# Kernel optimization log

Hardware: AMD Instinct MI355X
Metric: run time of the kernel (lower is better)

Reference implementation:

```python
import jax, jax.numpy as jnp
import numpy as np

D_MODEL = 512
D_K = 64
D_V = 128
H = D_MODEL // D_V  # 4 heads (num_head = d_model // d_v per the source)
B, N = 4, 2048


def setup_inputs() -> dict:
    key = jax.random.key(0)
    k0, k1, k2, k3, k4 = jax.random.split(key, 5)
    s = 0.02
    return {
        "input_x": jax.random.normal(k0, (B, N, D_MODEL), jnp.float32),
        "Wq": jax.random.normal(k1, (D_MODEL, H * D_K), jnp.float32) * s,
        "Wk": jax.random.normal(k2, (D_MODEL, H * D_K), jnp.float32) * s,
        "Wv": jax.random.normal(k3, (D_MODEL, D_MODEL), jnp.float32) * s,
        "Wo": jax.random.normal(k4, (D_MODEL, D_MODEL), jnp.float32) * s,
    }


def reference(input_x, Wq, Wk, Wv, Wo):
    b, n, _ = input_x.shape
    # Contiguous per-head slices in the source == a simple reshape here.
    q = (input_x @ Wq).reshape(b, n, H, D_K)   # [B,N,H,dk]
    k = (input_x @ Wk).reshape(b, n, H, D_K)   # [B,N,H,dk]
    v = (input_x @ Wv).reshape(b, n, H, D_V)   # [B,N,H,dv]
    scale = jnp.sqrt(jnp.float32(D_K))
    scores = jnp.einsum('bqhd,bkhd->bhqk', q, k) / scale  # [B,H,N,N]
    # FAITHFUL quirk: the source uses nn.Softmax() with no dim on a 3D
    # (B,N,N) tensor; PyTorch's legacy dim inference picks dim=0 (batch).
    attn = jax.nn.softmax(scores, axis=0)
    out = jnp.einsum('bhqk,bkhd->bqhd', attn, v).reshape(b, n, H * D_V)
    return out @ Wo
```

## Files before the change

kernel.cpp:

```cpp
#include <hip/hip_runtime.h>
#include <hip/hip_bf16.h>


typedef __attribute__((ext_vector_type(8))) short short8;
typedef __attribute__((ext_vector_type(4))) float floatx4;
typedef unsigned short u16;
typedef unsigned int u32;

#define MFMA16(a, b, c) __builtin_amdgcn_mfma_f32_16x16x32_bf16((a), (b), (c), 0, 0, 0)

__device__ __forceinline__ u16 f2bf(float f) {
    union { float f; unsigned u; } v; v.f = f;
    unsigned r = v.u + 0x7fffu + ((v.u >> 16) & 1u);
    return (u16)(r >> 16);
}

__device__ __forceinline__ float bf2f(u16 b) {
    union { unsigned u; float f; } v; v.u = ((u32)b) << 16;
    return v.f;
}

__device__ __forceinline__ u32 pk2bf(float a, float b) {
#if __has_builtin(__builtin_amdgcn_cvt_pk_bf16_f32)
    typedef __attribute__((ext_vector_type(2))) __bf16 bf16x2;
    union { bf16x2 v; u32 u; } c;
    c.v = __builtin_amdgcn_cvt_pk_bf16_f32(a, b);
    return c.u;
#else
    return (u32)f2bf(a) | ((u32)f2bf(b) << 16);
#endif
}

__device__ __forceinline__ float ex2(float x) {
#if __has_builtin(__builtin_amdgcn_exp2f)
    return __builtin_amdgcn_exp2f(x);
#else
    return exp2f(x);
#endif
}

__device__ __forceinline__ void gload_lds16(const u16* g, u16* l) {
    __builtin_amdgcn_global_load_lds(
        (const __attribute__((address_space(1))) void*)(const void*)g,
        (__attribute__((address_space(3))) void*)(void*)l, 16, 0, 0);
}

__global__ __launch_bounds__(256) void prep_all_kernel(
    const float* __restrict__ x, u16* __restrict__ xb,
    const float* __restrict__ Wq, const float* __restrict__ Wk,
    const float* __restrict__ Wv, const float* __restrict__ Wo,
    u16* __restrict__ WallT, u16* __restrict__ WoT) {
    int bid = blockIdx.x;
    if (bid < 4096) {
        int i = bid * 256 + threadIdx.x;
        float4 v = ((const float4*)x)[i];
        ushort4 o;
        o.x = f2bf(v.x); o.y = f2bf(v.y); o.z = f2bf(v.z); o.w = f2bf(v.w);
        ((ushort4*)xb)[i] = o;
        return;
    }
    int i = (bid - 4096) * 256 + threadIdx.x;
    if (i < 524288) {
        int n = i >> 9, k = i & 511;
        float v;
        if (n < 256)      v = Wq[k * 256 + n] * 0.18033688011f;
        else if (n < 512) v = Wk[k * 256 + (n - 256)];
        else              v = Wv[k * 512 + (n - 512)];
        WallT[i] = f2bf(v);
    } else {
        int j = i - 524288;
        int n = j >> 9, k = j & 511;
        WoT[j] = f2bf(Wo[k * 512 + n]);
    }
}

__global__ __launch_bounds__(512) void gemm_qkv_kernel(
    const u16* __restrict__ A, const u16* __restrict__ BT,
    u16* __restrict__ Qp, u16* __restrict__ Kp, u16* __restrict__ Vp,
    int Kdim) {
    __shared__ u16 sm[16896];
    u16* Asl = sm;
    u16* Bsl = sm + 8192;
    const int tid = threadIdx.x;
    const int bid0 = blockIdx.y * 8 + blockIdx.x;
    const int xcd = bid0 & 7, jj = bid0 >> 3;
    const int mbase = (xcd * 8 + (jj >> 3)) * 128;
    const int nbase = (jj & 7) * 128;
    const int wave = tid >> 6, lane = tid & 63;
    const int wm = wave >> 2, wn = wave & 3;
    const int lq = lane & 15, quad = lane >> 4;

    const u16* gA = A + (size_t)(mbase + wave * 16 + (lane >> 3)) * Kdim + (lane & 7) * 8;
    const u16* gB = BT + (size_t)(nbase + wave * 16 + (lane >> 3)) * Kdim + (lane & 7) * 8;
    u16* lA = &Asl[(wave * 16) * 64];
    u16* lB = &Bsl[(wave * 16) * 64];

    const floatx4 z4 = {0.f, 0.f, 0.f, 0.f};
    floatx4 acc[4][2];
#pragma unroll
    for (int i = 0; i < 4; i++)
#pragma unroll
        for (int j = 0; j < 2; j++) acc[i][j] = z4;

    const int nk = Kdim >> 6;
    for (int kk = 0; kk < nk; kk++) {
        const int kb = kk << 6;
        if (kk) __syncthreads();
#pragma unroll
        for (int i = 0; i < 2; i++) {
            gload_lds16(gA + kb + (size_t)(i * 8) * Kdim, lA + (i * 8) * 64);
            gload_lds16(gB + kb + (size_t)(i * 8) * Kdim, lB + (i * 8) * 64);
        }
        __syncthreads();
#pragma unroll
        for (int ki = 0; ki < 2; ki++) {
            short8 af[4], bf[2];
#pragma unroll
            for (int mi = 0; mi < 4; mi++)
                af[mi] = *(const short8*)&Asl[(wm * 64 + mi * 16 + lq) * 64 + ki * 32 + quad * 8];
#pragma unroll
            for (int ni = 0; ni < 2; ni++)
                bf[ni] = *(const short8*)&Bsl[(wn * 32 + ni * 16 + lq) * 64 + ki * 32 + quad * 8];
#pragma unroll
            for (int mi = 0; mi < 4; mi++)
#pragma unroll
                for (int ni = 0; ni < 2; ni++)
                    acc[mi][ni] = MFMA16(af[mi], bf[ni], acc[mi][ni]);
        }
    }
    __syncthreads();
    const bool vtile = (nbase >= 512);
#pragma unroll
    for (int mi = 0; mi < 4; mi++)
#pragma unroll
        for (int ni = 0; ni < 2; ni++) {
            int cl = wn * 32 + ni * 16 + lq;
#pragma unroll
            for (int r = 0; r < 4; r++) {
                int rl = wm * 64 + mi * 16 + quad * 4 + r;
                if (vtile) sm[cl * 132 + rl] = f2bf(acc[mi][ni][r]);
                else       sm[rl * 132 + cl] = f2bf(acc[mi][ni][r]);
            }
        }
    __syncthreads();
    const int b = mbase >> 11;
    const int keyb = mbase & 2047;
    if (nbase < 256) {
        const int hq = nbase >> 6;
        const int qs_base = keyb >> 4;
#pragma unroll
        for (int t = 0; t < 4; t++) {
            int l = wave * 4 + t;
            int qs2 = l >> 2, h2 = (l >> 1) & 1, ki = l & 1;
            int qd = lane >> 4, lqq = lane & 15;
            short8 v = *(const short8*)&sm[(qs2 * 16 + lqq) * 132 + h2 * 64 + ki * 32 + qd * 8];
            int h = hq + h2;
            size_t base = ((size_t)(((b * 4 + h) * 128 + (qs_base + qs2)) * 2 + ki) * 64 + lane) << 3;
            *(short8*)&Qp[base] = v;
        }
    } else if (nbase < 512) {
        const int hb = (nbase - 256) >> 6;
        const int ktb = keyb >> 6;
#pragma unroll
        for (int t = 0; t < 4; t++) {
            int l = wave * 4 + t;
            int kt2 = l >> 4, hf = (l >> 3) & 1, nj = (l >> 2) & 1;
            int h2 = (l >> 1) & 1, ki = l & 1;
            int quadk = lane >> 4, lqk = lane & 15;
            short8 v = *(const short8*)&sm[(kt2 * 64 + hf * 32 + lqk * 2 + nj) * 132 +
                                           h2 * 64 + ki * 32 + quadk * 8];
            int h = hb + h2;
            size_t base = ((size_t)(((((b * 4 + h) * 32 + (ktb + kt2)) * 2 + hf) * 2 + nj)
                                    * 2 + ki) * 64 + lane) << 3;
            *(short8*)&Kp[base] = v;
        }
    } else {
        const int h = (nbase - 512) >> 7;
        const int ktb = keyb >> 6;
#pragma unroll
        for (int t = 0; t < 4; t++) {
            int l = wave * 4 + t;
            int kt2 = l >> 4, hf = (l >> 3) & 1, niv = (l >> 1) & 3, wv = l & 1;
            int quadv = lane >> 4, lqv = lane & 15;
            short8 v = *(const short8*)&sm[(hf * 64 + niv * 16 + lqv) * 132 +
                                           kt2 * 64 + wv * 32 + quadv * 8];
            size_t base = ((size_t)(((((b * 4 + h) * 32 + (ktb + kt2)) * 2 + hf) * 4 + niv)
                                    * 2 + wv) * 64 + lane) << 3;
            *(short8*)&Vp[base] = v;
        }
    }
}

__global__ __launch_bounds__(512) void gemm_out_kernel(
    const u16* __restrict__ A, const u16* __restrict__ BT,
    float* __restrict__ Cf, int Kdim, int ldc) {
    __shared__ u16 Asl[64 * 64];
    __shared__ u16 Bsl[128 * 64];
    const int tid = threadIdx.x;
    const int bid0 = blockIdx.y * 4 + blockIdx.x;
    const int xcd = bid0 & 7, jj = bid0 >> 3;
    const int mbase = (xcd * 16 + (jj >> 2)) * 64;
    const int nbase = (jj & 3) * 128;
    const int wave = tid >> 6, lane = tid & 63;
    const int wm = wave >> 2, wn = wave & 3;
    const int lq = lane & 15, quad = lane >> 4;
    const size_t S = (size_t)8192 * 512;

    const u16* gA = A + (size_t)(mbase + wave * 8 + (lane >> 3)) * Kdim + (lane & 7) * 8;
    const u16* gB = BT + (size_t)(nbase + wave * 16 + (lane >> 3)) * Kdim + (lane & 7) * 8;
    u16* lAw = &Asl[(wave * 8 + (lane >> 3)) * 64 + (lane & 7) * 8];
    u16* lB = &Bsl[(wave * 16) * 64];

    const floatx4 z4 = {0.f, 0.f, 0.f, 0.f};
    floatx4 acc[2][2];
#pragma unroll
    for (int i = 0; i < 2; i++)
#pragma unroll
        for (int j = 0; j < 2; j++) acc[i][j] = z4;

    const int nk = Kdim >> 6;
    for (int kk = 0; kk < nk; kk++) {
        const int kb = kk << 6;
        short8 p0 = *(const short8*)(gA + kb);
        short8 p1 = *(const short8*)(gA + kb + S);
        short8 p2 = *(const short8*)(gA + kb + 2 * S);
        short8 p3 = *(const short8*)(gA + kb + 3 * S);
        if (kk) __syncthreads();
        gload_lds16(gB + kb, lB);
        gload_lds16(gB + kb + (size_t)8 * Kdim, lB + 8 * 64);
        short8 o;
#pragma unroll
        for (int j2 = 0; j2 < 8; j2++) {
            float s = bf2f((u16)p0[j2]) + bf2f((u16)p1[j2]) +
                      bf2f((u16)p2[j2]) + bf2f((u16)p3[j2]);
            o[j2] = (short)f2bf(s);
        }
        *(short8*)lAw = o;
        __syncthreads();
#pragma unroll
        for (int ki = 0; ki < 2; ki++) {
            short8 af[2], bf[2];
#pragma unroll
            for (int mi = 0; mi < 2; mi++)
                af[mi] = *(const short8*)&Asl[(wm * 32 + mi * 16 + lq) * 64 + ki * 32 + quad * 8];
#pragma unroll
            for (int ni = 0; ni < 2; ni++)
                bf[ni] = *(const short8*)&Bsl[(wn * 32 + ni * 16 + lq) * 64 + ki * 32 + quad * 8];
#pragma unroll
            for (int mi = 0; mi < 2; mi++)
#pragma unroll
                for (int ni = 0; ni < 2; ni++)
                    acc[mi][ni] = MFMA16(af[mi], bf[ni], acc[mi][ni]);
        }
    }
#pragma unroll
    for (int mi = 0; mi < 2; mi++)
#pragma unroll
        for (int ni = 0; ni < 2; ni++)
#pragma unroll
            for (int r = 0; r < 4; r++)
                Cf[(size_t)(mbase + wm * 32 + mi * 16 + quad * 4 + r) * ldc +
                   (nbase + wn * 32 + ni * 16 + lq)] = acc[mi][ni][r];
}

__global__ __launch_bounds__(512) void attn_kernel(const u16* __restrict__ Qp,
                                                   const u16* __restrict__ Kp,
                                                   const u16* __restrict__ Vp,
                                                   u16* __restrict__ Pp) {
    __shared__ u16 pl[2 * 4 * 4096];
    const int bx = blockIdx.x;
    const int xcd = bx & 7;
    const int j8 = bx >> 3;
    const int sl = xcd * 2 + (j8 >> 5);
    const int h = sl & 3;
    const int ck = sl >> 2;
    const int qt = j8 & 31;
    const int tid = threadIdx.x;
    const int wave = tid >> 6, lane = tid & 63;
    const int mi = wave & 3, half = wave >> 2;
    const int dq = wave;
    const int half_v = dq >> 2, ni_v = dq & 3;
    const int lq = lane & 15, quad = lane >> 4;
    const int qs = qt * 4 + mi;

    short8 aq[4][2];
#pragma unroll
    for (int b = 0; b < 4; b++)
#pragma unroll
        for (int ki = 0; ki < 2; ki++)
            aq[b][ki] = *(const short8*)&Qp[
                ((size_t)((((b * 4 + h) * 128 + qs) * 2 + ki) * 64 + lane) << 3)];

    const floatx4 z4 = {0.f, 0.f, 0.f, 0.f};
    floatx4 oacc[4][4];
#pragma unroll
    for (int b = 0; b < 4; b++)
#pragma unroll
        for (int m2 = 0; m2 < 4; m2++) oacc[b][m2] = z4;

    for (int kt = ck * 8; kt < ck * 8 + 8; kt++) {
        u16* plb = &pl[((kt & 1) * 4 + mi) * 4096];
        u16* plbuf = &pl[(kt & 1) * 4 * 4096];
        floatx4 s[4][2];
        __builtin_amdgcn_s_setprio(1);
#pragma unroll
        for (int b = 0; b < 4; b++) {
            const u16* kb = Kp +
                ((size_t)((((b * 4 + h) * 32 + kt) * 2 + half) * 2) << 10) +
                lane * 8;
#pragma unroll
            for (int nj = 0; nj < 2; nj++) {
                s[b][nj] = z4;
#pragma unroll
                for (int ki = 0; ki < 2; ki++)
                    s[b][nj] = MFMA16(aq[b][ki],
                                      *(const short8*)(kb + (nj * 2 + ki) * 512),
                                      s[b][nj]);
            }
        }
        __builtin_amdgcn_s_setprio(0);
        short8 vf[4][2];
#pragma unroll
        for (int b = 0; b < 4; b++) {
            const u16* vb = Vp +
                ((size_t)(((((b * 4 + h) * 32 + kt) * 2 + half_v) * 4 + ni_v) * 2) << 9) +
                lane * 8;
            vf[b][0] = *(const short8*)vb;
            vf[b][1] = *(const short8*)(vb + 512);
        }
#pragma unroll
        for (int r = 0; r < 4; r++) {
            float e0a = ex2(s[0][0][r]), e0b = ex2(s[0][1][r]);
            float e1a = ex2(s[1][0][r]), e1b = ex2(s[1][1][r]);
            float e2a = ex2(s[2][0][r]), e2b = ex2(s[2][1][r]);
            float e3a = ex2(s[3][0][r]), e3b = ex2(s[3][1][r]);
            float ia = __builtin_amdgcn_rcpf(e0a + e1a + e2a + e3a);
            float ib = __builtin_amdgcn_rcpf(e0b + e1b + e2b + e3b);
            int q = quad * 4 + r;
            int col = (half * 32 + 2 * lq) ^ ((q & 7) * 8);
            *(u32*)&plb[(0 * 16 + q) * 64 + col] = pk2bf(e0a * ia, e0b * ib);
            *(u32*)&plb[(1 * 16 + q) * 64 + col] = pk2bf(e1a * ia, e1b * ib);
            *(u32*)&plb[(2 * 16 + q) * 64 + col] = pk2bf(e2a * ia, e2b * ib);
            *(u32*)&plb[(3 * 16 + q) * 64 + col] = pk2bf(e3a * ia, e3b * ib);
        }
        __syncthreads();
        const int sw = (lq & 7) * 8;
        __builtin_amdgcn_s_setprio(1);
#pragma unroll
        for (int b = 0; b < 4; b++) {
#pragma unroll
            for (int m2 = 0; m2 < 4; m2++) {
                const u16* pm = plbuf + m2 * 4096;
                short8 ap0 = *(const short8*)&pm[(b * 16 + lq) * 64 + ((quad * 8) ^ sw)];
                short8 ap1 = *(const short8*)&pm[(b * 16 + lq) * 64 + ((32 + quad * 8) ^ sw)];
                oacc[b][m2] = MFMA16(ap0, vf[b][0], oacc[b][m2]);
                oacc[b][m2] = MFMA16(ap1, vf[b][1], oacc[b][m2]);
            }
        }
        __builtin_amdgcn_s_setprio(0);
    }
    u16* Pc = Pp + (size_t)ck * (8192 * 512);
#pragma unroll
    for (int b = 0; b < 4; b++)
#pragma unroll
        for (int m2 = 0; m2 < 4; m2++)
#pragma unroll
            for (int r = 0; r < 4; r++)
                Pc[(size_t)(b * 2048 + qt * 64 + m2 * 16 + quad * 4 + r) * 512 +
                   h * 128 + dq * 16 + lq] = f2bf(oacc[b][m2][r]);
}

extern "C" void kernel_launch(void* const* d_in, const int* in_sizes, int n_in,
                              void* d_out, int out_size, void* d_ws, size_t ws_size,
                              hipStream_t stream) {
    const float* x  = (const float*)d_in[0];
    const float* Wq = (const float*)d_in[1];
    const float* Wk = (const float*)d_in[2];
    const float* Wv = (const float*)d_in[3];
    const float* Wo = (const float*)d_in[4];
    float* out = (float*)d_out;

    char* ws = (char*)d_ws;
    u16* Pp    = (u16*)ws;
    u16* Xb    = (u16*)ws;
    u16* WallT = (u16*)(ws + (size_t)8 * 1024 * 1024);
    char* tail = ws + (size_t)32 * 1024 * 1024;
    u16* WoT   = (u16*)tail; tail += (size_t)512 * 512 * 2;
    u16* Qp    = (u16*)tail; tail += (size_t)8192 * 256 * 2;
    u16* Kp    = (u16*)tail; tail += (size_t)8192 * 256 * 2;
    u16* Vp    = (u16*)tail; tail += (size_t)8192 * 512 * 2;

    prep_all_kernel<<<7168, 256, 0, stream>>>(x, Xb, Wq, Wk, Wv, Wo, WallT, WoT);
    gemm_qkv_kernel<<<dim3(8, 64), 512, 0, stream>>>(Xb, WallT, Qp, Kp, Vp, 512);
    attn_kernel<<<512, 512, 0, stream>>>(Qp, Kp, Vp, Pp);
    gemm_out_kernel<<<dim3(4, 128), 512, 0, stream>>>(Pp, WoT, out, 512, 512);
}
```

Baseline: 165.5 us.

## Double-buffer LDS in QKV and output GEMMs, simplify attention block mapping

Both GEMM kernels now keep two LDS stages, so the global-to-LDS loads for the next K tile are issued before the MFMAs on the current tile, leaving one barrier per iteration. In the output GEMM the four-way sum of partial results is also prefetched into registers and written to the other buffer after compute. The attention kernel drops its XCD-aware block remapping and the s_setprio hints. The extra LDS raises shared memory per block, which may reduce occupancy, and the simpler mapping may hurt L2 locality.

```diff
diff --git a/kernel.cpp b/kernel.cpp
--- a/kernel.cpp
+++ b/kernel.cpp
@@ -78,9 +78,7 @@
     const u16* __restrict__ A, const u16* __restrict__ BT,
     u16* __restrict__ Qp, u16* __restrict__ Kp, u16* __restrict__ Vp,
     int Kdim) {
-    __shared__ u16 sm[16896];
-    u16* Asl = sm;
-    u16* Bsl = sm + 8192;
+    __shared__ u16 sm[32768];
     const int tid = threadIdx.x;
     const int bid0 = blockIdx.y * 8 + blockIdx.x;
     const int xcd = bid0 & 7, jj = bid0 >> 3;
@@ -92,8 +90,6 @@
 
     const u16* gA = A + (size_t)(mbase + wave * 16 + (lane >> 3)) * Kdim + (lane & 7) * 8;
     const u16* gB = BT + (size_t)(nbase + wave * 16 + (lane >> 3)) * Kdim + (lane & 7) * 8;
-    u16* lA = &Asl[(wave * 16) * 64];
-    u16* lB = &Bsl[(wave * 16) * 64];
 
     const floatx4 z4 = {0.f, 0.f, 0.f, 0.f};
     floatx4 acc[4][2];
@@ -102,33 +98,44 @@
 #pragma unroll
         for (int j = 0; j < 2; j++) acc[i][j] = z4;
 
+#pragma unroll
+    for (int i = 0; i < 2; i++) {
+        gload_lds16(gA + (size_t)(i * 8) * Kdim, sm + (wave * 16 + i * 8) * 64);
+        gload_lds16(gB + (size_t)(i * 8) * Kdim, sm + 8192 + (wave * 16 + i * 8) * 64);
+    }
+    __syncthreads();
+
     const int nk = Kdim >> 6;
     for (int kk = 0; kk < nk; kk++) {
-        const int kb = kk << 6;
-        if (kk) __syncthreads();
-#pragma unroll
-        for (int i = 0; i < 2; i++) {
-            gload_lds16(gA + kb + (size_t)(i * 8) * Kdim, lA + (i * 8) * 64);
-            gload_lds16(gB + kb + (size_t)(i * 8) * Kdim, lB + (i * 8) * 64);
-        }
-        __syncthreads();
+        const int ph = kk & 1;
+        if (kk + 1 < nk) {
+            const int kb = (kk + 1) << 6;
+            u16* dst = sm + (ph ^ 1) * 16384;
+#pragma unroll
+            for (int i = 0; i < 2; i++) {
+                gload_lds16(gA + kb + (size_t)(i * 8) * Kdim, dst + (wave * 16 + i * 8) * 64);
+                gload_lds16(gB + kb + (size_t)(i * 8) * Kdim, dst + 8192 + (wave * 16 + i * 8) * 64);
+            }
+        }
+        const u16* As = sm + ph * 16384;
+        const u16* Bs = As + 8192;
 #pragma unroll
         for (int ki = 0; ki < 2; ki++) {
             short8 af[4], bf[2];
 #pragma unroll
             for (int mi = 0; mi < 4; mi++)
-                af[mi] = *(const short8*)&Asl[(wm * 64 + mi * 16 + lq) * 64 + ki * 32 + quad * 8];
+                af[mi] = *(const short8*)&As[(wm * 64 + mi * 16 + lq) * 64 + ki * 32 + quad * 8];
 #pragma unroll
             for (int ni = 0; ni < 2; ni++)
-                bf[ni] = *(const short8*)&Bsl[(wn * 32 + ni * 16 + lq) * 64 + ki * 32 + quad * 8];
+                bf[ni] = *(const short8*)&Bs[(wn * 32 + ni * 16 + lq) * 64 + ki * 32 + quad * 8];
 #pragma unroll
             for (int mi = 0; mi < 4; mi++)
 #pragma unroll
                 for (int ni = 0; ni < 2; ni++)
                     acc[mi][ni] = MFMA16(af[mi], bf[ni], acc[mi][ni]);
         }
-    }
-    __syncthreads();
+        __syncthreads();
+    }
     const bool vtile = (nbase >= 512);
 #pragma unroll
     for (int mi = 0; mi < 4; mi++)
@@ -194,8 +201,8 @@
 __global__ __launch_bounds__(512) void gemm_out_kernel(
     const u16* __restrict__ A, const u16* __restrict__ BT,
     float* __restrict__ Cf, int Kdim, int ldc) {
-    __shared__ u16 Asl[64 * 64];
-    __shared__ u16 Bsl[128 * 64];
+    __shared__ u16 Asl[2 * 4096];
+    __shared__ u16 Bsl[2 * 8192];
     const int tid = threadIdx.x;
     const int bid0 = blockIdx.y * 4 + blockIdx.x;
     const int xcd = bid0 & 7, jj = bid0 >> 3;
@@ -208,8 +215,8 @@
 
     const u16* gA = A + (size_t)(mbase + wave * 8 + (lane >> 3)) * Kdim + (lane & 7) * 8;
     const u16* gB = BT + (size_t)(nbase + wave * 16 + (lane >> 3)) * Kdim + (lane & 7) * 8;
-    u16* lAw = &Asl[(wave * 8 + (lane >> 3)) * 64 + (lane & 7) * 8];
-    u16* lB = &Bsl[(wave * 16) * 64];
+    const int lAoff = (wave * 8 + (lane >> 3)) * 64 + (lane & 7) * 8;
+    const int lBoff = (wave * 16) * 64;
 
     const floatx4 z4 = {0.f, 0.f, 0.f, 0.f};
     floatx4 acc[2][2];
@@ -218,16 +225,13 @@
 #pragma unroll
         for (int j = 0; j < 2; j++) acc[i][j] = z4;
 
-    const int nk = Kdim >> 6;
-    for (int kk = 0; kk < nk; kk++) {
-        const int kb = kk << 6;
-        short8 p0 = *(const short8*)(gA + kb);
-        short8 p1 = *(const short8*)(gA + kb + S);
-        short8 p2 = *(const short8*)(gA + kb + 2 * S);
-        short8 p3 = *(const short8*)(gA + kb + 3 * S);
-        if (kk) __syncthreads();
-        gload_lds16(gB + kb, lB);
-        gload_lds16(gB + kb + (size_t)8 * Kdim, lB + 8 * 64);
+    {
+        short8 p0 = *(const short8*)(gA);
+        short8 p1 = *(const short8*)(gA + S);
+        short8 p2 = *(const short8*)(gA + 2 * S);
+        short8 p3 = *(const short8*)(gA + 3 * S);
+        gload_lds16(gB, Bsl + lBoff);
+        gload_lds16(gB + (size_t)8 * Kdim, Bsl + lBoff + 8 * 64);
         short8 o;
 #pragma unroll
         for (int j2 = 0; j2 < 8; j2++) {
@@ -235,23 +239,53 @@
                       bf2f((u16)p2[j2]) + bf2f((u16)p3[j2]);
             o[j2] = (short)f2bf(s);
         }
-        *(short8*)lAw = o;
-        __syncthreads();
+        *(short8*)&Asl[lAoff] = o;
+    }
+    __syncthreads();
+
+    const int nk = Kdim >> 6;
+    for (int kk = 0; kk < nk; kk++) {
+        const int ph = kk & 1;
+        short8 p0, p1, p2, p3;
+        const bool more = (kk + 1 < nk);
+        if (more) {
+            const int kbn = (kk + 1) << 6;
+            p0 = *(const short8*)(gA + kbn);
+            p1 = *(const short8*)(gA + kbn + S);
+            p2 = *(const short8*)(gA + kbn + 2 * S);
+            p3 = *(const short8*)(gA + kbn + 3 * S);
+            u16* dB = Bsl + (ph ^ 1) * 8192 + lBoff;
+            gload_lds16(gB + kbn, dB);
+            gload_lds16(gB + kbn + (size_t)8 * Kdim, dB + 8 * 64);
+        }
+        const u16* As = Asl + ph * 4096;
+        const u16* Bs = Bsl + ph * 8192;
 #pragma unroll
         for (int ki = 0; ki < 2; ki++) {
             short8 af[2], bf[2];
 #pragma unroll
             for (int mi = 0; mi < 2; mi++)
-                af[mi] = *(const short8*)&Asl[(wm * 32 + mi * 16 + lq) * 64 + ki * 32 + quad * 8];
+                af[mi] = *(const short8*)&As[(wm * 32 + mi * 16 + lq) * 64 + ki * 32 + quad * 8];
 #pragma unroll
             for (int ni = 0; ni < 2; ni++)
-                bf[ni] = *(const short8*)&Bsl[(wn * 32 + ni * 16 + lq) * 64 + ki * 32 + quad * 8];
+                bf[ni] = *(const short8*)&Bs[(wn * 32 + ni * 16 + lq) * 64 + ki * 32 + quad * 8];
 #pragma unroll
             for (int mi = 0; mi < 2; mi++)
 #pragma unroll
                 for (int ni = 0; ni < 2; ni++)
                     acc[mi][ni] = MFMA16(af[mi], bf[ni], acc[mi][ni]);
         }
+        if (more) {
+            short8 o;
+#pragma unroll
+            for (int j2 = 0; j2 < 8; j2++) {
+                float s = bf2f((u16)p0[j2]) + bf2f((u16)p1[j2]) +
+                          bf2f((u16)p2[j2]) + bf2f((u16)p3[j2]);
+                o[j2] = (short)f2bf(s);
+            }
+            *(short8*)&Asl[(ph ^ 1) * 4096 + lAoff] = o;
+        }
+        __syncthreads();
     }
 #pragma unroll
     for (int mi = 0; mi < 2; mi++)
@@ -269,12 +303,9 @@
                                                    u16* __restrict__ Pp) {
     __shared__ u16 pl[2 * 4 * 4096];
     const int bx = blockIdx.x;
-    const int xcd = bx & 7;
-    const int j8 = bx >> 3;
-    const int sl = xcd * 2 + (j8 >> 5);
-    const int h = sl & 3;
-    const int ck = sl >> 2;
-    const int qt = j8 & 31;
+    const int h = bx & 3;
+    const int ck = (bx >> 2) & 3;
+    const int qt = bx >> 4;
     const int tid = threadIdx.x;
     const int wave = tid >> 6, lane = tid & 63;
     const int mi = wave & 3, half = wave >> 2;
@@ -302,7 +333,6 @@
         u16* plb = &pl[((kt & 1) * 4 + mi) * 4096];
         u16* plbuf = &pl[(kt & 1) * 4 * 4096];
         floatx4 s[4][2];
-        __builtin_amdgcn_s_setprio(1);
 #pragma unroll
         for (int b = 0; b < 4; b++) {
             const u16* kb = Kp +
@@ -318,7 +348,6 @@
                                       s[b][nj]);
             }
         }
-        __builtin_amdgcn_s_setprio(0);
         short8 vf[4][2];
 #pragma unroll
         for (int b = 0; b < 4; b++) {
@@ -345,7 +374,6 @@
         }
         __syncthreads();
         const int sw = (lq & 7) * 8;
-        __builtin_amdgcn_s_setprio(1);
 #pragma unroll
         for (int b = 0; b < 4; b++) {
 #pragma unroll
@@ -357,7 +385,6 @@
                 oacc[b][m2] = MFMA16(ap1, vf[b][1], oacc[b][m2]);
             }
         }
-        __builtin_amdgcn_s_setprio(0);
     }
     u16* Pc = Pp + (size_t)ck * (8192 * 512);
 #pragma unroll
```

After: 165.1 us. No clear change (-0.2%).

## Shrink output GEMM tile to 64x64, drop setprio, simplify attention block mapping

Applied to the files above, without the earlier changes.

The output projection GEMM moves from 64x128 tiles with 512 threads to 64x64 tiles with 256 threads and twice as many blocks. Each thread now reduces two rows of the four split-K partial sums. The attention kernel drops its s_setprio hints and uses a plain block-to-(head, chunk, query-tile) mapping instead of the XCD-aware swizzle. These are separate tuning changes: more, smaller GEMM blocks for occupancy, at the cost of re-reading the A partials twice as often and losing L2 locality across XCDs in attention.

```diff
diff --git a/kernel.cpp b/kernel.cpp
--- a/kernel.cpp
+++ b/kernel.cpp
@@ -191,25 +191,25 @@
     }
 }
 
-__global__ __launch_bounds__(512) void gemm_out_kernel(
+__global__ __launch_bounds__(256) void gemm_out_kernel(
     const u16* __restrict__ A, const u16* __restrict__ BT,
     float* __restrict__ Cf, int Kdim, int ldc) {
     __shared__ u16 Asl[64 * 64];
-    __shared__ u16 Bsl[128 * 64];
+    __shared__ u16 Bsl[64 * 64];
     const int tid = threadIdx.x;
-    const int bid0 = blockIdx.y * 4 + blockIdx.x;
+    const int bid0 = blockIdx.y * 8 + blockIdx.x;
     const int xcd = bid0 & 7, jj = bid0 >> 3;
-    const int mbase = (xcd * 16 + (jj >> 2)) * 64;
-    const int nbase = (jj & 3) * 128;
+    const int mbase = (xcd * 16 + (jj >> 3)) * 64;
+    const int nbase = (jj & 7) * 64;
     const int wave = tid >> 6, lane = tid & 63;
-    const int wm = wave >> 2, wn = wave & 3;
+    const int wm = wave >> 1, wn = wave & 1;
     const int lq = lane & 15, quad = lane >> 4;
     const size_t S = (size_t)8192 * 512;
 
-    const u16* gA = A + (size_t)(mbase + wave * 8 + (lane >> 3)) * Kdim + (lane & 7) * 8;
+    const u16* gA = A + (size_t)(mbase + wave * 16 + (lane >> 3)) * Kdim + (lane & 7) * 8;
     const u16* gB = BT + (size_t)(nbase + wave * 16 + (lane >> 3)) * Kdim + (lane & 7) * 8;
-    u16* lAw = &Asl[(wave * 8 + (lane >> 3)) * 64 + (lane & 7) * 8];
-    u16* lB = &Bsl[(wave * 16) * 64];
+    const int lAoff = (wave * 16 + (lane >> 3)) * 64 + (lane & 7) * 8;
+    const int lBoff = (wave * 16) * 64;
 
     const floatx4 z4 = {0.f, 0.f, 0.f, 0.f};
     floatx4 acc[2][2];
@@ -221,21 +221,30 @@
     const int nk = Kdim >> 6;
     for (int kk = 0; kk < nk; kk++) {
         const int kb = kk << 6;
-        short8 p0 = *(const short8*)(gA + kb);
-        short8 p1 = *(const short8*)(gA + kb + S);
-        short8 p2 = *(const short8*)(gA + kb + 2 * S);
-        short8 p3 = *(const short8*)(gA + kb + 3 * S);
+        short8 pa0 = *(const short8*)(gA + kb);
+        short8 pa1 = *(const short8*)(gA + kb + S);
+        short8 pa2 = *(const short8*)(gA + kb + 2 * S);
+        short8 pa3 = *(const short8*)(gA + kb + 3 * S);
+        const u16* gA1 = gA + kb + (size_t)8 * Kdim;
+        short8 pb0 = *(const short8*)(gA1);
+        short8 pb1 = *(const short8*)(gA1 + S);
+        short8 pb2 = *(const short8*)(gA1 + 2 * S);
+        short8 pb3 = *(const short8*)(gA1 + 3 * S);
         if (kk) __syncthreads();
-        gload_lds16(gB + kb, lB);
-        gload_lds16(gB + kb + (size_t)8 * Kdim, lB + 8 * 64);
-        short8 o;
+        gload_lds16(gB + kb, Bsl + lBoff);
+        gload_lds16(gB + kb + (size_t)8 * Kdim, Bsl + lBoff + 8 * 64);
+        short8 oa, ob;
 #pragma unroll
         for (int j2 = 0; j2 < 8; j2++) {
-            float s = bf2f((u16)p0[j2]) + bf2f((u16)p1[j2]) +
-                      bf2f((u16)p2[j2]) + bf2f((u16)p3[j2]);
-            o[j2] = (short)f2bf(s);
-        }
-        *(short8*)lAw = o;
+            float sa = bf2f((u16)pa0[j2]) + bf2f((u16)pa1[j2]) +
+                       bf2f((u16)pa2[j2]) + bf2f((u16)pa3[j2]);
+            oa[j2] = (short)f2bf(sa);
+            float sb = bf2f((u16)pb0[j2]) + bf2f((u16)pb1[j2]) +
+                       bf2f((u16)pb2[j2]) + bf2f((u16)pb3[j2]);
+            ob[j2] = (short)f2bf(sb);
+        }
+        *(short8*)&Asl[lAoff] = oa;
+        *(short8*)&Asl[lAoff + 8 * 64] = ob;
         __syncthreads();
 #pragma unroll
         for (int ki = 0; ki < 2; ki++) {
@@ -269,12 +278,9 @@
                                                    u16* __restrict__ Pp) {
     __shared__ u16 pl[2 * 4 * 4096];
     const int bx = blockIdx.x;
-    const int xcd = bx & 7;
-    const int j8 = bx >> 3;
-    const int sl = xcd * 2 + (j8 >> 5);
-    const int h = sl & 3;
-    const int ck = sl >> 2;
-    const int qt = j8 & 31;
+    const int h = bx & 3;
+    const int ck = (bx >> 2) & 3;
+    const int qt = bx >> 4;
     const int tid = threadIdx.x;
     const int wave = tid >> 6, lane = tid & 63;
     const int mi = wave & 3, half = wave >> 2;
@@ -302,7 +308,6 @@
         u16* plb = &pl[((kt & 1) * 4 + mi) * 4096];
         u16* plbuf = &pl[(kt & 1) * 4 * 4096];
         floatx4 s[4][2];
-        __builtin_amdgcn_s_setprio(1);
 #pragma unroll
         for (int b = 0; b < 4; b++) {
             const u16* kb = Kp +
@@ -318,7 +323,6 @@
                                       s[b][nj]);
             }
         }
-        __builtin_amdgcn_s_setprio(0);
         short8 vf[4][2];
 #pragma unroll
         for (int b = 0; b < 4; b++) {
@@ -345,7 +349,6 @@
         }
         __syncthreads();
         const int sw = (lq & 7) * 8;
-        __builtin_amdgcn_s_setprio(1);
 #pragma unroll
         for (int b = 0; b < 4; b++) {
 #pragma unroll
@@ -357,7 +360,6 @@
                 oacc[b][m2] = MFMA16(ap1, vf[b][1], oacc[b][m2]);
             }
         }
-        __builtin_amdgcn_s_setprio(0);
     }
     u16* Pc = Pp + (size_t)ck * (8192 * 512);
 #pragma unroll
@@ -393,5 +395,5 @@
     prep_all_kernel<<<7168, 256, 0, stream>>>(x, Xb, Wq, Wk, Wv, Wo, WallT, WoT);
     gemm_qkv_kernel<<<dim3(8, 64), 512, 0, stream>>>(Xb, WallT, Qp, Kp, Vp, 512);
     attn_kernel<<<512, 512, 0, stream>>>(Qp, Kp, Vp, Pp);
-    gemm_out_kernel<<<dim3(4, 128), 512, 0, stream>>>(Pp, WoT, out, 512, 512);
-}
+    gemm_out_kernel<<<dim3(8, 128), 256, 0, stream>>>(Pp, WoT, out, 512, 512);
+}
```

Result: no change. 163.7 us (-1.1%).

## Tile weight transpose through LDS, simplify attention block mapping, drop setprio

Applied to the files above, without the earlier changes.

The weight-prep kernel now transposes the weights in 64x64 tiles through LDS. Each tile is read with coalesced float4 loads and written back with 16-byte stores, replacing the old strided per-element gather, and this cuts the prep grid from 7168 to 4288 blocks. Separately, the attention kernel drops its XCD-aware block-to-(head, chunk, query-tile) remapping in favour of a plain linear mapping. It also removes the s_setprio hints around its MFMA sections. The mapping change may alter L2 locality of K/V reads across XCDs, and removing the priority hints may change how waves interleave.

```diff
diff --git a/kernel.cpp b/kernel.cpp
--- a/kernel.cpp
+++ b/kernel.cpp
@@ -50,27 +50,43 @@
     const float* __restrict__ Wq, const float* __restrict__ Wk,
     const float* __restrict__ Wv, const float* __restrict__ Wo,
     u16* __restrict__ WallT, u16* __restrict__ WoT) {
-    int bid = blockIdx.x;
+    const int bid = blockIdx.x;
+    const int tid = threadIdx.x;
     if (bid < 4096) {
-        int i = bid * 256 + threadIdx.x;
+        int i = bid * 256 + tid;
         float4 v = ((const float4*)x)[i];
         ushort4 o;
         o.x = f2bf(v.x); o.y = f2bf(v.y); o.z = f2bf(v.z); o.w = f2bf(v.w);
         ((ushort4*)xb)[i] = o;
         return;
     }
-    int i = (bid - 4096) * 256 + threadIdx.x;
-    if (i < 524288) {
-        int n = i >> 9, k = i & 511;
-        float v;
-        if (n < 256)      v = Wq[k * 256 + n] * 0.18033688011f;
-        else if (n < 512) v = Wk[k * 256 + (n - 256)];
-        else              v = Wv[k * 512 + (n - 512)];
-        WallT[i] = f2bf(v);
-    } else {
-        int j = i - 524288;
-        int n = j >> 9, k = j & 511;
-        WoT[j] = f2bf(Wo[k * 512 + n]);
+    __shared__ u16 lds[64 * 80];
+    const int t = bid - 4096;
+    const int k0 = (t & 7) * 64;
+    const int n0 = (t >> 3) * 64;
+    const float* src; int ld, coff; float scale = 1.0f;
+    u16* dst;
+    if (n0 < 256)       { src = Wq; ld = 256; coff = n0;        dst = WallT + (size_t)n0 * 512; scale = 0.18033688011f; }
+    else if (n0 < 512)  { src = Wk; ld = 256; coff = n0 - 256;  dst = WallT + (size_t)n0 * 512; }
+    else if (n0 < 1024) { src = Wv; ld = 512; coff = n0 - 512;  dst = WallT + (size_t)n0 * 512; }
+    else                { src = Wo; ld = 512; coff = n0 - 1024; dst = WoT + (size_t)(n0 - 1024) * 512; }
+#pragma unroll
+    for (int p = 0; p < 4; p++) {
+        int r  = (tid >> 4) + p * 16;
+        int c4 = (tid & 15) * 4;
+        float4 v = *(const float4*)&src[(size_t)(k0 + r) * ld + coff + c4];
+        lds[(c4 + 0) * 80 + r] = f2bf(v.x * scale);
+        lds[(c4 + 1) * 80 + r] = f2bf(v.y * scale);
+        lds[(c4 + 2) * 80 + r] = f2bf(v.z * scale);
+        lds[(c4 + 3) * 80 + r] = f2bf(v.w * scale);
+    }
+    __syncthreads();
+#pragma unroll
+    for (int p = 0; p < 2; p++) {
+        int nn = (tid >> 3) + p * 32;
+        int kk = (tid & 7) * 8;
+        *(short8*)&dst[(size_t)(n0 >= 1024 ? nn : nn) * 0 +
+                       (size_t)(nn) * 512 + k0 + kk] = *(const short8*)&lds[nn * 80 + kk];
     }
 }
 
@@ -269,12 +285,9 @@
                                                    u16* __restrict__ Pp) {
     __shared__ u16 pl[2 * 4 * 4096];
     const int bx = blockIdx.x;
-    const int xcd = bx & 7;
-    const int j8 = bx >> 3;
-    const int sl = xcd * 2 + (j8 >> 5);
-    const int h = sl & 3;
-    const int ck = sl >> 2;
-    const int qt = j8 & 31;
+    const int h = bx & 3;
+    const int ck = (bx >> 2) & 3;
+    const int qt = bx >> 4;
     const int tid = threadIdx.x;
     const int wave = tid >> 6, lane = tid & 63;
     const int mi = wave & 3, half = wave >> 2;
@@ -302,7 +315,6 @@
         u16* plb = &pl[((kt & 1) * 4 + mi) * 4096];
         u16* plbuf = &pl[(kt & 1) * 4 * 4096];
         floatx4 s[4][2];
-        __builtin_amdgcn_s_setprio(1);
 #pragma unroll
         for (int b = 0; b < 4; b++) {
             const u16* kb = Kp +
@@ -318,7 +330,6 @@
                                       s[b][nj]);
             }
         }
-        __builtin_amdgcn_s_setprio(0);
         short8 vf[4][2];
 #pragma unroll
         for (int b = 0; b < 4; b++) {
@@ -345,7 +356,6 @@
         }
         __syncthreads();
         const int sw = (lq & 7) * 8;
-        __builtin_amdgcn_s_setprio(1);
 #pragma unroll
         for (int b = 0; b < 4; b++) {
 #pragma unroll
@@ -357,7 +367,6 @@
                 oacc[b][m2] = MFMA16(ap1, vf[b][1], oacc[b][m2]);
             }
         }
-        __builtin_amdgcn_s_setprio(0);
     }
     u16* Pc = Pp + (size_t)ck * (8192 * 512);
 #pragma unroll
@@ -390,7 +399,7 @@
     u16* Kp    = (u16*)tail; tail += (size_t)8192 * 256 * 2;
     u16* Vp    = (u16*)tail; tail += (size_t)8192 * 512 * 2;
 
-    prep_all_kernel<<<7168, 256, 0, stream>>>(x, Xb, Wq, Wk, Wv, Wo, WallT, WoT);
+    prep_all_kernel<<<4288, 256, 0, stream>>>(x, Xb, Wq, Wk, Wv, Wo, WallT, WoT);
     gemm_qkv_kernel<<<dim3(8, 64), 512, 0, stream>>>(Xb, WallT, Qp, Kp, Vp, 512);
     attn_kernel<<<512, 512, 0, stream>>>(Qp, Kp, Vp, Pp);
     gemm_out_kernel<<<dim3(4, 128), 512, 0, stream>>>(Pp, WoT, out, 512, 512);
```

New measurement: 164.0 us. No clear change (-0.9%).
